# Kernel optimization log

Hardware: AMD Instinct MI355X
Metric: run time of the kernel (lower is better)

Reference implementation:

```python
import jax, jax.numpy as jnp
import numpy as np

N, F, O, E = 2048, 128, 128, 16


def setup_inputs() -> dict:
    key = jax.random.key(0)
    ks = jax.random.split(key, 6)
    x = jax.random.normal(ks[0], (N, F), dtype=jnp.float32)
    # two supports (normalized adjacency-like dense matrices)
    support = jax.random.uniform(ks[1], (2, N, N), dtype=jnp.float32)
    edge_feature = jax.random.normal(ks[2], (N, N, E), dtype=jnp.float32)
    # glorot-ish scale for edge weight and dense weights
    weight_edge = jax.random.normal(ks[3], (N, N, E), dtype=jnp.float32) * 0.05
    bias_edge = jnp.zeros((N, N), dtype=jnp.float32)
    glorot = float(np.sqrt(6.0 / (F + O)))
    w0 = jax.random.uniform(ks[4], (F, O), dtype=jnp.float32, minval=-glorot, maxval=glorot)
    w1 = jax.random.uniform(ks[5], (F, O), dtype=jnp.float32, minval=-glorot, maxval=glorot)
    b = jnp.zeros((O,), dtype=jnp.float32)
    return {"x": x, "support": support, "edge_feature": edge_feature,
            "weight_edge": weight_edge, "bias_edge": bias_edge,
            "w0": w0, "w1": w1, "b": b}


def reference(x, support, edge_feature, weight_edge, bias_edge, w0, w1, b):
    # support branch 0: plain GCN propagation  (SpMM expressed dense)
    pre0 = x @ w0                      # [N, O]
    s0 = support[0] @ pre0             # [N, O]
    # support branch 1: edge-feature gated propagation
    pre1 = x @ w1                      # [N, O]
    # per-pair dot of edge features with per-pair weights -> [N, N] gate
    edge = jax.nn.sigmoid(jnp.einsum('nme,nme->nm', edge_feature, weight_edge) + bias_edge)
    s1 = (edge * support[1]) @ pre1    # gated adjacency matmul, [N, O]
    out = s0 + s1 + b                  # add_n + bias
    return jax.nn.relu(out)
```

## Files before the change

kernel.cpp:

```cpp
#include <hip/hip_runtime.h>
#include <math.h>

#define N 2048
#define F 128
#define O 128
#define E 16

typedef __attribute__((ext_vector_type(8))) short    shortx8;
typedef __attribute__((ext_vector_type(8))) unsigned short u16x8;
typedef __attribute__((ext_vector_type(4))) float    floatx4;

static __device__ __forceinline__ unsigned short f2bf(float f) {
    unsigned int u = __float_as_uint(f);
    unsigned int r = (u + 0x7FFFu + ((u >> 16) & 1u)) >> 16;
    return (unsigned short)r;
}

__global__ __launch_bounds__(128)
void pre_gemm(const float* __restrict__ x,
              const float* __restrict__ w0,
              const float* __restrict__ w1,
              unsigned short* __restrict__ pre_bf) {
    const int n = blockIdx.x;
    const int b = blockIdx.y;
    const int o = threadIdx.x;
    const float* __restrict__ w = b ? w1 : w0;
    __shared__ float xs[F];
    xs[o] = x[(size_t)n * F + o];
    __syncthreads();
    float acc = 0.f;
#pragma unroll 8
    for (int k = 0; k < F; ++k)
        acc += xs[k] * w[(size_t)k * O + o];
    pre_bf[(size_t)b * N * O + (size_t)n * O + o] = f2bf(acc);
}

__global__ __launch_bounds__(256)
void transpose_pre(const unsigned short* __restrict__ pre_bf,
                   unsigned short* __restrict__ preT) {
    __shared__ unsigned short tile[64][65];
    const int n0 = blockIdx.x * 64, o0 = blockIdx.y * 64;
    const size_t base = (size_t)blockIdx.z * N * O;
    const int t = threadIdx.x;
    const int r = t >> 2, q = t & 3;
    const unsigned short* src = pre_bf + base + (size_t)(n0 + r) * O + o0 + q * 16;
    u16x8 v0 = *(const u16x8*)(src);
    u16x8 v1 = *(const u16x8*)(src + 8);
#pragma unroll
    for (int j = 0; j < 8; ++j) {
        tile[q * 16 + j][r]     = v0[j];
        tile[q * 16 + 8 + j][r] = v1[j];
    }
    __syncthreads();
    u16x8 w0v, w1v;
#pragma unroll
    for (int j = 0; j < 8; ++j) {
        w0v[j] = tile[r][q * 16 + j];
        w1v[j] = tile[r][q * 16 + 8 + j];
    }
    unsigned short* dst = preT + base + (size_t)(o0 + r) * N + n0 + q * 16;
    *(u16x8*)(dst)     = w0v;
    *(u16x8*)(dst + 8) = w1v;
}

#define BN 32
#define MK 512
#define BK 32
#define BPAD 48

__global__ __launch_bounds__(512)
void fused_gemm(const float* __restrict__ sup,
                const float* __restrict__ ef,
                const float* __restrict__ we,
                const float* __restrict__ be,
                const unsigned short* __restrict__ preT,
                float* __restrict__ partial) {
    __shared__ unsigned short s0A[BN * BK];
    __shared__ unsigned short gA [BN * BK];
    __shared__ unsigned short B0 [O * BPAD];
    __shared__ unsigned short B1 [O * BPAD];

    const int tid = threadIdx.x;
    const int bx  = blockIdx.x;
    const int rb  = bx & 63;
    const int kc  = bx >> 6;
    const int n0      = rb * BN;
    const int m_base  = kc * MK;

    const float* __restrict__ S0   = sup;
    const float* __restrict__ sup1 = sup + (size_t)N * N;

    const int lane = tid & 63;
    const int wid  = tid >> 6;
    const int wrow = wid >> 2;
    const int wcol = wid & 3;

    const int nn0 = tid >> 5;
    const int mm0 = tid & 31;
    const int bo = tid >> 2;
    const int bq = tid & 3;

    floatx4 acc0 = {0.f, 0.f, 0.f, 0.f};
    floatx4 acc1 = {0.f, 0.f, 0.f, 0.f};

    for (int step = 0; step < MK / BK; ++step) {
        const int m0 = m_base + step * BK;

        {
            const size_t src = (size_t)bo * N + (size_t)(m0 + bq * 8);
            u16x8 v0 = *(const u16x8*)(preT + src);
            u16x8 v1 = *(const u16x8*)(preT + (size_t)O * N + src);
            *(u16x8*)(B0 + bo * BPAD + bq * 8) = v0;
            *(u16x8*)(B1 + bo * BPAD + bq * 8) = v1;
        }

#pragma unroll
        for (int rep = 0; rep < 2; ++rep) {
            const int nn = nn0 + rep * 16;
            const size_t pix = (size_t)(n0 + nn) * N + (size_t)(m0 + mm0);
            const float4* e4 = (const float4*)(ef + pix * E);
            const float4* w4 = (const float4*)(we + pix * E);
            float v = 0.f;
#pragma unroll
            for (int j = 0; j < 4; ++j) {
                const float4 a = e4[j], b = w4[j];
                v += a.x * b.x + a.y * b.y + a.z * b.z + a.w * b.w;
            }
            const float tt = v + be[pix];
            const float g  = (1.f / (1.f + __expf(-tt))) * sup1[pix];
            gA [nn * BK + mm0] = f2bf(g);
            s0A[nn * BK + mm0] = f2bf(S0[pix]);
        }
        __syncthreads();

        {
            const int arow = wrow * 16 + (lane & 15);
            const int kg   = lane >> 4;
            const shortx8 a_s = *(const shortx8*)(s0A + arow * BK + kg * 8);
            const shortx8 a_g = *(const shortx8*)(gA  + arow * BK + kg * 8);
            const int col0 = wcol * 32 + (lane & 15);
            const shortx8 b00 = *(const shortx8*)(B0 + col0 * BPAD + kg * 8);
            const shortx8 b10 = *(const shortx8*)(B1 + col0 * BPAD + kg * 8);
            const shortx8 b01 = *(const shortx8*)(B0 + (col0 + 16) * BPAD + kg * 8);
            const shortx8 b11 = *(const shortx8*)(B1 + (col0 + 16) * BPAD + kg * 8);
            acc0 = __builtin_amdgcn_mfma_f32_16x16x32_bf16(a_s, b00, acc0, 0, 0, 0);
            acc0 = __builtin_amdgcn_mfma_f32_16x16x32_bf16(a_g, b10, acc0, 0, 0, 0);
            acc1 = __builtin_amdgcn_mfma_f32_16x16x32_bf16(a_s, b01, acc1, 0, 0, 0);
            acc1 = __builtin_amdgcn_mfma_f32_16x16x32_bf16(a_g, b11, acc1, 0, 0, 0);
        }
        __syncthreads();
    }

    const int prow = (lane >> 4) * 4;
    const int pcol = wcol * 32 + (lane & 15);
    float* dst = partial + (size_t)kc * (N * O)
               + (size_t)(n0 + wrow * 16 + prow) * O + pcol;
#pragma unroll
    for (int j = 0; j < 4; ++j) {
        dst[(size_t)j * O]      = acc0[j];
        dst[(size_t)j * O + 16] = acc1[j];
    }
}

__global__ __launch_bounds__(256)
void reduce_out(const float* __restrict__ partial,
                const float* __restrict__ bias,
                float* __restrict__ out) {
    const int i4 = blockIdx.x * 256 + threadIdx.x;
    const float4* p = (const float4*)partial;
    const float4 a = p[i4];
    const float4 b = p[i4 + 65536];
    const float4 c = p[i4 + 2 * 65536];
    const float4 d = p[i4 + 3 * 65536];
    const float4 bb = ((const float4*)bias)[i4 & 31];
    float4 r;
    r.x = fmaxf(a.x + b.x + c.x + d.x + bb.x, 0.f);
    r.y = fmaxf(a.y + b.y + c.y + d.y + bb.y, 0.f);
    r.z = fmaxf(a.z + b.z + c.z + d.z + bb.z, 0.f);
    r.w = fmaxf(a.w + b.w + c.w + d.w + bb.w, 0.f);
    ((float4*)out)[i4] = r;
}

extern "C" void kernel_launch(void* const* d_in, const int* in_sizes, int n_in,
                              void* d_out, int out_size, void* d_ws, size_t ws_size,
                              hipStream_t stream) {
    const float* x   = (const float*)d_in[0];
    const float* sup = (const float*)d_in[1];
    const float* ef  = (const float*)d_in[2];
    const float* we  = (const float*)d_in[3];
    const float* be  = (const float*)d_in[4];
    const float* w0  = (const float*)d_in[5];
    const float* w1  = (const float*)d_in[6];
    const float* b   = (const float*)d_in[7];
    float* out = (float*)d_out;

    unsigned short* pre_bf = (unsigned short*)d_ws;
    unsigned short* preT   = pre_bf + 2 * (size_t)N * O;
    float* partial = (float*)(preT + 2 * (size_t)N * O);

    pre_gemm<<<dim3(N, 2), 128, 0, stream>>>(x, w0, w1, pre_bf);
    transpose_pre<<<dim3(N / 64, O / 64, 2), 256, 0, stream>>>(pre_bf, preT);
    fused_gemm<<<256, 512, 0, stream>>>(sup, ef, we, be, preT, partial);
    reduce_out<<<256, 256, 0, stream>>>(partial, b, out);
}
```

Before: 161.4 us.

## Double-buffer fused gemm with register prefetch and raise K-split to 8

Restructures the fused gate+GEMM kernel to prefetch the next step's edge features, weights, supports and preT slices into registers while the MFMAs run on the current LDS buffer. Adds a second set of LDS buffers so production of one stage overlaps consumption of the other. Raises the K-split from 4 to 8 chunks, doubling the grid to 512 blocks for more memory parallelism, and adjusts LDS padding. The reduction now sums 8 partials, which adds partial-buffer traffic, and the register prefetch raises register pressure.

```diff
diff --git a/kernel.cpp b/kernel.cpp
--- a/kernel.cpp
+++ b/kernel.cpp
@@ -6,9 +6,17 @@
 #define O 128
 #define E 16
 
-typedef __attribute__((ext_vector_type(8))) short    shortx8;
+#define BN 32
+#define BK 32
+#define KC 8
+#define MK (N / KC)
+#define STEPS (MK / BK)
+#define APAD 40
+#define BPAD 40
+
+typedef __attribute__((ext_vector_type(8))) short          shortx8;
 typedef __attribute__((ext_vector_type(8))) unsigned short u16x8;
-typedef __attribute__((ext_vector_type(4))) float    floatx4;
+typedef __attribute__((ext_vector_type(4))) float          floatx4;
 
 static __device__ __forceinline__ unsigned short f2bf(float f) {
     unsigned int u = __float_as_uint(f);
@@ -63,29 +71,95 @@
     *(u16x8*)(dst + 8) = w1v;
 }
 
-#define BN 32
-#define MK 512
-#define BK 32
-#define BPAD 48
-
-__global__ __launch_bounds__(512)
+
+struct Pref {
+    float4 e0[4], e1[4], w0[4], w1[4];
+    float  be0, be1, s00, s01, s10, s11;
+    u16x8  bv0, bv1;
+};
+
+__device__ __forceinline__ void load_step(
+    const float* __restrict__ ef, const float* __restrict__ we,
+    const float* __restrict__ be, const float* __restrict__ S0,
+    const float* __restrict__ sup1, const unsigned short* __restrict__ preT,
+    size_t pix0, size_t sbase, int m0, Pref& P)
+{
+    const size_t pixA = pix0 + (size_t)m0;
+    const size_t pixB = pixA + (size_t)16 * N;
+    const float4* eA = (const float4*)(ef + pixA * E);
+    const float4* wA = (const float4*)(we + pixA * E);
+    const float4* eB = (const float4*)(ef + pixB * E);
+    const float4* wB = (const float4*)(we + pixB * E);
+#pragma unroll
+    for (int j = 0; j < 4; ++j) {
+        P.e0[j] = eA[j]; P.w0[j] = wA[j];
+        P.e1[j] = eB[j]; P.w1[j] = wB[j];
+    }
+    P.be0 = be[pixA]; P.s00 = S0[pixA]; P.s10 = sup1[pixA];
+    P.be1 = be[pixB]; P.s01 = S0[pixB]; P.s11 = sup1[pixB];
+    const size_t src = sbase + (size_t)m0;
+    P.bv0 = *(const u16x8*)(preT + src);
+    P.bv1 = *(const u16x8*)(preT + (size_t)O * N + src);
+}
+
+__device__ __forceinline__ void produce(
+    const Pref& P, int nn0, int mm0, int bo, int bq,
+    unsigned short* aS, unsigned short* aG,
+    unsigned short* B0, unsigned short* B1)
+{
+    float v0 = 0.f, v1 = 0.f;
+#pragma unroll
+    for (int j = 0; j < 4; ++j) {
+        v0 += P.e0[j].x * P.w0[j].x + P.e0[j].y * P.w0[j].y
+            + P.e0[j].z * P.w0[j].z + P.e0[j].w * P.w0[j].w;
+        v1 += P.e1[j].x * P.w1[j].x + P.e1[j].y * P.w1[j].y
+            + P.e1[j].z * P.w1[j].z + P.e1[j].w * P.w1[j].w;
+    }
+    const float g0 = (1.f / (1.f + __expf(-(v0 + P.be0)))) * P.s10;
+    const float g1 = (1.f / (1.f + __expf(-(v1 + P.be1)))) * P.s11;
+    aG[nn0 * APAD + mm0]        = f2bf(g0);
+    aG[(nn0 + 16) * APAD + mm0] = f2bf(g1);
+    aS[nn0 * APAD + mm0]        = f2bf(P.s00);
+    aS[(nn0 + 16) * APAD + mm0] = f2bf(P.s01);
+    *(u16x8*)(B0 + bo * BPAD + bq * 8) = P.bv0;
+    *(u16x8*)(B1 + bo * BPAD + bq * 8) = P.bv1;
+}
+
+__device__ __forceinline__ void mfma_step(
+    const unsigned short* aS, const unsigned short* aG,
+    const unsigned short* B0, const unsigned short* B1,
+    int arow, int kg, int col0, floatx4& acc0, floatx4& acc1)
+{
+    const shortx8 a_s = *(const shortx8*)(aS + arow * APAD + kg * 8);
+    const shortx8 a_g = *(const shortx8*)(aG + arow * APAD + kg * 8);
+    const shortx8 b00 = *(const shortx8*)(B0 + col0 * BPAD + kg * 8);
+    const shortx8 b10 = *(const shortx8*)(B1 + col0 * BPAD + kg * 8);
+    const shortx8 b01 = *(const shortx8*)(B0 + (col0 + 16) * BPAD + kg * 8);
+    const shortx8 b11 = *(const shortx8*)(B1 + (col0 + 16) * BPAD + kg * 8);
+    acc0 = __builtin_amdgcn_mfma_f32_16x16x32_bf16(a_s, b00, acc0, 0, 0, 0);
+    acc0 = __builtin_amdgcn_mfma_f32_16x16x32_bf16(a_g, b10, acc0, 0, 0, 0);
+    acc1 = __builtin_amdgcn_mfma_f32_16x16x32_bf16(a_s, b01, acc1, 0, 0, 0);
+    acc1 = __builtin_amdgcn_mfma_f32_16x16x32_bf16(a_g, b11, acc1, 0, 0, 0);
+}
+
+__global__ __launch_bounds__(512, 4)
 void fused_gemm(const float* __restrict__ sup,
                 const float* __restrict__ ef,
                 const float* __restrict__ we,
                 const float* __restrict__ be,
                 const unsigned short* __restrict__ preT,
                 float* __restrict__ partial) {
-    __shared__ unsigned short s0A[BN * BK];
-    __shared__ unsigned short gA [BN * BK];
-    __shared__ unsigned short B0 [O * BPAD];
-    __shared__ unsigned short B1 [O * BPAD];
+    __shared__ unsigned short aS0[BN * APAD], aG0[BN * APAD];
+    __shared__ unsigned short B00[O * BPAD],  B10[O * BPAD];
+    __shared__ unsigned short aS1[BN * APAD], aG1[BN * APAD];
+    __shared__ unsigned short B01[O * BPAD],  B11[O * BPAD];
 
     const int tid = threadIdx.x;
     const int bx  = blockIdx.x;
     const int rb  = bx & 63;
     const int kc  = bx >> 6;
-    const int n0      = rb * BN;
-    const int m_base  = kc * MK;
+    const int n0     = rb * BN;
+    const int m_base = kc * MK;
 
     const float* __restrict__ S0   = sup;
     const float* __restrict__ sup1 = sup + (size_t)N * N;
@@ -97,57 +171,38 @@
 
     const int nn0 = tid >> 5;
     const int mm0 = tid & 31;
-    const int bo = tid >> 2;
-    const int bq = tid & 3;
+    const int bo  = tid >> 2;
+    const int bq  = tid & 3;
+
+    const size_t pix0  = (size_t)(n0 + nn0) * N + (size_t)(m_base + mm0);
+    const size_t sbase = (size_t)bo * N + (size_t)(m_base + bq * 8);
+
+    const int arow = wrow * 16 + (lane & 15);
+    const int kg   = lane >> 4;
+    const int col0 = wcol * 32 + (lane & 15);
 
     floatx4 acc0 = {0.f, 0.f, 0.f, 0.f};
     floatx4 acc1 = {0.f, 0.f, 0.f, 0.f};
 
-    for (int step = 0; step < MK / BK; ++step) {
-        const int m0 = m_base + step * BK;
-
-        {
-            const size_t src = (size_t)bo * N + (size_t)(m0 + bq * 8);
-            u16x8 v0 = *(const u16x8*)(preT + src);
-            u16x8 v1 = *(const u16x8*)(preT + (size_t)O * N + src);
-            *(u16x8*)(B0 + bo * BPAD + bq * 8) = v0;
-            *(u16x8*)(B1 + bo * BPAD + bq * 8) = v1;
+    Pref P;
+    load_step(ef, we, be, S0, sup1, preT, pix0, sbase, 0, P);
+    produce(P, nn0, mm0, bo, bq, aS0, aG0, B00, B10);
+    load_step(ef, we, be, S0, sup1, preT, pix0, sbase, BK, P);
+    __syncthreads();
+
+#pragma unroll 1
+    for (int s = 0; s < STEPS; s += 2) {
+        produce(P, nn0, mm0, bo, bq, aS1, aG1, B01, B11);
+        if (s + 2 < STEPS)
+            load_step(ef, we, be, S0, sup1, preT, pix0, sbase, (s + 2) * BK, P);
+        mfma_step(aS0, aG0, B00, B10, arow, kg, col0, acc0, acc1);
+        __syncthreads();
+        if (s + 2 < STEPS) {
+            produce(P, nn0, mm0, bo, bq, aS0, aG0, B00, B10);
+            if (s + 3 < STEPS)
+                load_step(ef, we, be, S0, sup1, preT, pix0, sbase, (s + 3) * BK, P);
         }
-
-#pragma unroll
-        for (int rep = 0; rep < 2; ++rep) {
-            const int nn = nn0 + rep * 16;
-            const size_t pix = (size_t)(n0 + nn) * N + (size_t)(m0 + mm0);
-            const float4* e4 = (const float4*)(ef + pix * E);
-            const float4* w4 = (const float4*)(we + pix * E);
-            float v = 0.f;
-#pragma unroll
-            for (int j = 0; j < 4; ++j) {
-                const float4 a = e4[j], b = w4[j];
-                v += a.x * b.x + a.y * b.y + a.z * b.z + a.w * b.w;
-            }
-            const float tt = v + be[pix];
-            const float g  = (1.f / (1.f + __expf(-tt))) * sup1[pix];
-            gA [nn * BK + mm0] = f2bf(g);
-            s0A[nn * BK + mm0] = f2bf(S0[pix]);
-        }
-        __syncthreads();
-
-        {
-            const int arow = wrow * 16 + (lane & 15);
-            const int kg   = lane >> 4;
-            const shortx8 a_s = *(const shortx8*)(s0A + arow * BK + kg * 8);
-            const shortx8 a_g = *(const shortx8*)(gA  + arow * BK + kg * 8);
-            const int col0 = wcol * 32 + (lane & 15);
-            const shortx8 b00 = *(const shortx8*)(B0 + col0 * BPAD + kg * 8);
-            const shortx8 b10 = *(const shortx8*)(B1 + col0 * BPAD + kg * 8);
-            const shortx8 b01 = *(const shortx8*)(B0 + (col0 + 16) * BPAD + kg * 8);
-            const shortx8 b11 = *(const shortx8*)(B1 + (col0 + 16) * BPAD + kg * 8);
-            acc0 = __builtin_amdgcn_mfma_f32_16x16x32_bf16(a_s, b00, acc0, 0, 0, 0);
-            acc0 = __builtin_amdgcn_mfma_f32_16x16x32_bf16(a_g, b10, acc0, 0, 0, 0);
-            acc1 = __builtin_amdgcn_mfma_f32_16x16x32_bf16(a_s, b01, acc1, 0, 0, 0);
-            acc1 = __builtin_amdgcn_mfma_f32_16x16x32_bf16(a_g, b11, acc1, 0, 0, 0);
-        }
+        mfma_step(aS1, aG1, B01, B11, arow, kg, col0, acc0, acc1);
         __syncthreads();
     }
 
@@ -168,17 +223,19 @@
                 float* __restrict__ out) {
     const int i4 = blockIdx.x * 256 + threadIdx.x;
     const float4* p = (const float4*)partial;
-    const float4 a = p[i4];
-    const float4 b = p[i4 + 65536];
-    const float4 c = p[i4 + 2 * 65536];
-    const float4 d = p[i4 + 3 * 65536];
+    float4 r = p[i4];
+#pragma unroll
+    for (int j = 1; j < KC; ++j) {
+        const float4 a = p[i4 + (size_t)j * 65536];
+        r.x += a.x; r.y += a.y; r.z += a.z; r.w += a.w;
+    }
     const float4 bb = ((const float4*)bias)[i4 & 31];
-    float4 r;
-    r.x = fmaxf(a.x + b.x + c.x + d.x + bb.x, 0.f);
-    r.y = fmaxf(a.y + b.y + c.y + d.y + bb.y, 0.f);
-    r.z = fmaxf(a.z + b.z + c.z + d.z + bb.z, 0.f);
-    r.w = fmaxf(a.w + b.w + c.w + d.w + bb.w, 0.f);
-    ((float4*)out)[i4] = r;
+    float4 o;
+    o.x = fmaxf(r.x + bb.x, 0.f);
+    o.y = fmaxf(r.y + bb.y, 0.f);
+    o.z = fmaxf(r.z + bb.z, 0.f);
+    o.w = fmaxf(r.w + bb.w, 0.f);
+    ((float4*)out)[i4] = o;
 }
 
 extern "C" void kernel_launch(void* const* d_in, const int* in_sizes, int n_in,
@@ -200,6 +257,6 @@
 
     pre_gemm<<<dim3(N, 2), 128, 0, stream>>>(x, w0, w1, pre_bf);
     transpose_pre<<<dim3(N / 64, O / 64, 2), 256, 0, stream>>>(pre_bf, preT);
-    fused_gemm<<<256, 512, 0, stream>>>(sup, ef, we, be, preT, partial);
+    fused_gemm<<<KC * 64, 512, 0, stream>>>(sup, ef, we, be, preT, partial);
     reduce_out<<<256, 256, 0, stream>>>(partial, b, out);
 }
```

Measured after the change: 148.6 us. -8.0%, faster.
